# Kernel tuning notes

Measured on AMD Instinct MI355X. Metric: run time of the kernel, lower is better.

## Reference

```python
import jax, jax.numpy as jnp
import numpy as np

NUM_HEADS = 16
NUM_EXPERTS = 8
TOP_K = 2
LN_EPS = 1e-5


def _layernorm(x, g, b):
    mu = x.mean(-1, keepdims=True)
    var = ((x - mu) ** 2).mean(-1, keepdims=True)
    return (x - mu) * jax.lax.rsqrt(var + LN_EPS) * g + b


def _rope(x, cos, sin):
    # x: [B,S,H,D]; cos/sin: [S, D//2]; interleaved even/odd pairs
    B, S, H, D = x.shape
    xr = x.reshape(B, S, H, D // 2, 2)
    xe, xo = xr[..., 0], xr[..., 1]
    c = cos[None, :, None, :]
    s = sin[None, :, None, :]
    ye = xe * c - xo * s
    yo = xe * s + xo * c
    return jnp.stack((ye, yo), axis=-1).reshape(B, S, H, D)


def setup_inputs() -> dict:
    key = jax.random.key(0)
    ks = jax.random.split(key, 8)
    B, S, D = 4, 512, 1024
    E, Hd = NUM_EXPERTS, 1792
    sc = 0.02
    return {
        'x': jax.random.normal(ks[0], (B, S, D), jnp.float32),
        'ln1_g': jnp.ones((D,), jnp.float32),
        'ln1_b': jnp.zeros((D,), jnp.float32),
        'ln2_g': jnp.ones((D,), jnp.float32),
        'ln2_b': jnp.zeros((D,), jnp.float32),
        'w_qkv': jax.random.normal(ks[1], (D, 3 * D), jnp.float32) * sc,
        'w_o': jax.random.normal(ks[2], (D, D), jnp.float32) * sc,
        'gate_w': jax.random.normal(ks[3], (D, E), jnp.float32) * sc,
        'w_gate': jax.random.normal(ks[4], (E, D, Hd), jnp.float32) * sc,
        'w_up': jax.random.normal(ks[5], (E, D, Hd), jnp.float32) * sc,
        'w_down': jax.random.normal(ks[6], (E, Hd, D), jnp.float32) * sc,
    }


def reference(x, ln1_g, ln1_b, ln2_g, ln2_b, w_qkv, w_o, gate_w, w_gate, w_up, w_down):
    B, S, D = x.shape
    H = NUM_HEADS
    hd = D // H

    # --- attention with RoPE ---
    xn = _layernorm(x, ln1_g, ln1_b)
    qkv = xn @ w_qkv                      # [B,S,3D]
    q, k, v = jnp.split(qkv, 3, axis=-1)
    q = q.reshape(B, S, H, hd)
    k = k.reshape(B, S, H, hd)
    v = v.reshape(B, S, H, hd)
    inv_freq = 1.0 / (10000.0 ** (jnp.arange(0, hd, 2, dtype=jnp.float32) / hd))
    t = jnp.arange(S, dtype=jnp.float32)
    freqs = jnp.outer(t, inv_freq)        # [S, hd//2]
    cos, sin = jnp.cos(freqs), jnp.sin(freqs)
    q = _rope(q, cos, sin)
    k = _rope(k, cos, sin)
    scale = 1.0 / jnp.sqrt(jnp.asarray(hd, x.dtype))
    scores = jnp.einsum('bshd,bthd->bhst', q, k) * scale
    causal = jnp.tril(jnp.ones((S, S), bool))
    scores = jnp.where(causal[None, None], scores, jnp.finfo(scores.dtype).min)
    attn = jax.nn.softmax(scores, axis=-1)
    attn_out = jnp.einsum('bhst,bthd->bshd', attn, v).reshape(B, S, D)
    x = x + attn_out @ w_o

    # --- MoE ---
    xn2 = _layernorm(x, ln2_g, ln2_b)
    xf = xn2.reshape(-1, D)               # [T, D]
    logits = (xf.astype(jnp.bfloat16) @ gate_w.astype(jnp.bfloat16)).astype(jnp.float32)
    topk_w, topk_i = jax.lax.top_k(logits, TOP_K)
    topk_w = jax.nn.softmax(topk_w, axis=-1)
    probs = jax.nn.softmax(logits, axis=-1)
    expert_dist = probs.mean(0)
    lb_loss = NUM_EXPERTS * (expert_dist ** 2).sum()
    # dense dispatch: combine weights [T,E], zero where not selected (same math as sort/gather/scatter)
    cw = (jax.nn.one_hot(topk_i, NUM_EXPERTS, dtype=xf.dtype) * topk_w[..., None].astype(xf.dtype)).sum(1)
    g = jnp.einsum('td,edh->teh', xf, w_gate)
    u = jnp.einsum('td,edh->teh', xf, w_up)
    h = jax.nn.silu(g) * u
    down = jnp.einsum('teh,ehd->ted', h, w_down)
    moe_out = jnp.einsum('ted,te->td', down, cw).reshape(B, S, D)
    x = x + moe_out
    return (x, lb_loss, expert_dist)
```

## Files before the change

### kernel.cpp

```cpp
#include <hip/hip_runtime.h>
#include <hip/hip_bf16.h>
#include <math.h>

#define B_    4
#define S_    512
#define D_    1024
#define T_    2048
#define H_    16
#define HD_   64
#define E_    8
#define HID_  1792
#define D3_   3072
#define GU_   (2 * HID_)

typedef unsigned short ushort_t;
typedef __bf16 bf16x8 __attribute__((ext_vector_type(8)));
typedef float  floatx4 __attribute__((ext_vector_type(4)));

__device__ inline float bf2f(ushort_t u) {
    return __uint_as_float(((unsigned)u) << 16);
}
__device__ inline ushort_t f2bf(float f) {
    __hip_bfloat16 h = __float2bfloat16(f);
    return __builtin_bit_cast(ushort_t, h);
}

__device__ __forceinline__ void gl2lds16(const ushort_t* g, ushort_t* l) {
    __builtin_amdgcn_global_load_lds(
        (const __attribute__((address_space(1))) void*)g,
        (__attribute__((address_space(3))) void*)l, 16, 0, 0);
}

__global__ __launch_bounds__(256) void transpose_bf16_kernel(
    const float* __restrict__ in, ushort_t* __restrict__ out,
    int R, int C, int mul, int add, long outEstride)
{
    __shared__ float tile[32][33];
    const int bx = blockIdx.x * 32;
    const int by = blockIdx.y * 32;
    const size_t iofs = (size_t)blockIdx.z * R * C;
    const size_t oofs = (size_t)blockIdx.z * outEstride;
    const int tx = threadIdx.x & 31;
    const int ty = threadIdx.x >> 5;
#pragma unroll
    for (int i = 0; i < 4; i++) {
        int r = by + ty + i * 8;
        tile[ty + i * 8][tx] = in[iofs + (size_t)r * C + bx + tx];
    }
    __syncthreads();
#pragma unroll
    for (int i = 0; i < 4; i++) {
        int c = bx + ty + i * 8;
        out[oofs + (size_t)(c * mul + add) * R + by + tx] = f2bf(tile[tx][ty + i * 8]);
    }
}

__global__ __launch_bounds__(256) void ln_kernel(
    const float* __restrict__ x, const float* __restrict__ g,
    const float* __restrict__ b, float* __restrict__ outf,
    ushort_t* __restrict__ outb)
{
    const int t = blockIdx.x;
    const int tid = threadIdx.x;
    const int wave = tid >> 6, lane = tid & 63;
    const float4 v = ((const float4*)(x + (size_t)t * D_))[tid];

    float s = v.x + v.y + v.z + v.w;
#pragma unroll
    for (int off = 32; off; off >>= 1) s += __shfl_xor(s, off);
    __shared__ float red1[4];
    __shared__ float red2[4];
    if (lane == 0) red1[wave] = s;
    __syncthreads();
    const float mu = (red1[0] + red1[1] + red1[2] + red1[3]) * (1.0f / D_);

    const float dx = v.x - mu, dy = v.y - mu, dz = v.z - mu, dw = v.w - mu;
    float vs = dx * dx + dy * dy + dz * dz + dw * dw;
#pragma unroll
    for (int off = 32; off; off >>= 1) vs += __shfl_xor(vs, off);
    if (lane == 0) red2[wave] = vs;
    __syncthreads();
    const float var = (red2[0] + red2[1] + red2[2] + red2[3]) * (1.0f / D_);
    const float rs = 1.0f / sqrtf(var + 1e-5f);

    const float4 gg = ((const float4*)g)[tid];
    const float4 bb = ((const float4*)b)[tid];
    float4 o;
    o.x = dx * rs * gg.x + bb.x;
    o.y = dy * rs * gg.y + bb.y;
    o.z = dz * rs * gg.z + bb.z;
    o.w = dw * rs * gg.w + bb.w;
    if (outf) ((float4*)(outf + (size_t)t * D_))[tid] = o;
    if (outb) {
        ushort4 ob;
        ob.x = f2bf(o.x); ob.y = f2bf(o.y); ob.z = f2bf(o.z); ob.w = f2bf(o.w);
        ((ushort4*)(outb + (size_t)t * D_))[tid] = ob;
    }
}

template<int TM>
__global__ __launch_bounds__(256) void sgemm_kernel(
    const float* __restrict__ A, const float* __restrict__ B,
    const float* __restrict__ res, float* __restrict__ C,
    int M, int N, int K)
{
    constexpr int RM  = TM / 16;
    constexpr int TPR = 256 / TM;
    constexpr int KF  = 16 / TPR;
    __shared__ float As[16][TM + 4];
    __shared__ float Bs[16][68];
    const int tid = threadIdx.x;
    const int m0 = blockIdx.y * TM, n0 = blockIdx.x * 64;
    const int tx = tid & 15, ty = tid >> 4;

    float acc[RM][4] = {};

    const int arow = tid / TPR;
    const int akk  = (tid % TPR) * KF;
    const int bk = tid >> 4;
    const int bc = (tid & 15) * 4;

    const float* Ap = A + (size_t)(m0 + arow) * K + akk;
    const float* Bp = B + (size_t)bk * N + n0 + bc;

    for (int k0 = 0; k0 < K; k0 += 16) {
        float av[KF];
#pragma unroll
        for (int f = 0; f < KF / 4; f++) {
            const float4 t = *(const float4*)(Ap + k0 + f * 4);
            av[f * 4 + 0] = t.x; av[f * 4 + 1] = t.y;
            av[f * 4 + 2] = t.z; av[f * 4 + 3] = t.w;
        }
        const float4 bv = *(const float4*)(Bp + (size_t)k0 * N);
        __syncthreads();
#pragma unroll
        for (int i = 0; i < KF; i++) As[akk + i][arow] = av[i];
        *(float4*)&Bs[bk][bc] = bv;
        __syncthreads();
#pragma unroll
        for (int k = 0; k < 16; k++) {
            float a[RM];
#pragma unroll
            for (int f = 0; f < RM / 4; f++) {
                const float4 t = *(const float4*)&As[k][ty * RM + f * 4];
                a[f * 4 + 0] = t.x; a[f * 4 + 1] = t.y;
                a[f * 4 + 2] = t.z; a[f * 4 + 3] = t.w;
            }
            const float4 bb = *(const float4*)&Bs[k][tx * 4];
            const float bj[4] = {bb.x, bb.y, bb.z, bb.w};
#pragma unroll
            for (int i = 0; i < RM; i++)
#pragma unroll
                for (int j = 0; j < 4; j++)
                    acc[i][j] = fmaf(a[i], bj[j], acc[i][j]);
        }
    }

#pragma unroll
    for (int i = 0; i < RM; i++) {
        const int row = m0 + ty * RM + i;
        const size_t base = (size_t)row * N + n0 + tx * 4;
        float4 o;
        o.x = acc[i][0]; o.y = acc[i][1]; o.z = acc[i][2]; o.w = acc[i][3];
        if (res) {
            const float4 r0 = *(const float4*)(res + base);
            o.x += r0.x; o.y += r0.y; o.z += r0.z; o.w += r0.w;
        }
        *(float4*)(C + base) = o;
    }
}

__global__ __launch_bounds__(256) void gateup_idx_kernel(
    const ushort_t* __restrict__ A, const ushort_t* __restrict__ Bgu,
    const int* __restrict__ cnt, const int* __restrict__ tok,
    ushort_t* __restrict__ Hc)
{
    const int e = blockIdx.z;
    const int cntE = cnt[e];
    const int row0 = blockIdx.y * 128;
    if (row0 >= cntE) return;
    const int col0 = blockIdx.x * 128;
    const ushort_t* Bt = Bgu + (size_t)e * GU_ * D_;
    ushort_t* Hp = Hc + (size_t)e * T_ * HID_;

    __shared__ __align__(16) ushort_t As[128 * 32];
    __shared__ __align__(16) ushort_t Bs[128 * 32];
    const int tid = threadIdx.x, w = tid >> 6, lane = tid & 63;
    const int lr = lane >> 2, lc = (lane & 3) * 8;
    const int wm = (w >> 1) * 64, wn = (w & 1) * 64;
    const int lm = lane & 15, lq = lane >> 4;

    floatx4 acc[4][4] = {};

    int r0c = row0 + w * 16 + lr;  if (r0c > cntE - 1) r0c = cntE - 1;
    int r1c = row0 + 64 + w * 16 + lr; if (r1c > cntE - 1) r1c = cntE - 1;
    const ushort_t* Ap0 = A + (size_t)tok[e * T_ + r0c] * D_ + lc;
    const ushort_t* Ap1 = A + (size_t)tok[e * T_ + r1c] * D_ + lc;
    const ushort_t* Bp = Bt + (size_t)(col0 + w * 16 + lr) * D_ + lc;
    ushort_t* lA = As + w * 512;
    ushort_t* lB = Bs + w * 512;

    for (int k0 = 0; k0 < D_; k0 += 32) {
        __syncthreads();
        gl2lds16(Ap0 + k0, lA);
        gl2lds16(Ap1 + k0, lA + 2048);
        gl2lds16(Bp + k0, lB);
        gl2lds16(Bp + k0 + (size_t)64 * D_, lB + 2048);
        __syncthreads();
        bf16x8 a[4], b[4];
#pragma unroll
        for (int i = 0; i < 4; i++)
            a[i] = *(const bf16x8*)(As + (wm + i * 16 + lm) * 32 + lq * 8);
#pragma unroll
        for (int j = 0; j < 4; j++)
            b[j] = *(const bf16x8*)(Bs + (wn + j * 16 + lm) * 32 + lq * 8);
#pragma unroll
        for (int i = 0; i < 4; i++)
#pragma unroll
            for (int j = 0; j < 4; j++)
                acc[i][j] = __builtin_amdgcn_mfma_f32_16x16x32_bf16(a[i], b[j], acc[i][j], 0, 0, 0);
    }

#pragma unroll
    for (int i = 0; i < 4; i++)
#pragma unroll
        for (int j = 0; j < 4; j++)
#pragma unroll
            for (int r = 0; r < 4; r++) {
                const float v = acc[i][j][r];
                const float vp = __shfl_xor(v, 1);
                const float g = (lm & 1) ? vp : v;
                const float u = (lm & 1) ? v : vp;
                const float h = g / (1.f + __expf(-g)) * u;
                if (!(lm & 1)) {
                    const int row = row0 + wm + i * 16 + lq * 4 + r;
                    const int col = col0 + wn + j * 16 + lm;
                    Hp[(size_t)row * HID_ + (col >> 1)] = f2bf(h);
                }
            }
}

__global__ __launch_bounds__(256) void down_idx_kernel(
    const ushort_t* __restrict__ Hc, const ushort_t* __restrict__ Wd,
    const int* __restrict__ cnt, const int* __restrict__ tok,
    const float* __restrict__ wt, float* __restrict__ out)
{
    const int e = blockIdx.z;
    const int cntE = cnt[e];
    const int row0 = blockIdx.y * 128;
    if (row0 >= cntE) return;
    const int col0 = blockIdx.x * 128;
    const ushort_t* A = Hc + (size_t)e * T_ * HID_;
    const ushort_t* Bt = Wd + (size_t)e * D_ * HID_;

    __shared__ __align__(16) ushort_t As[128 * 32];
    __shared__ __align__(16) ushort_t Bs[128 * 32];
    const int tid = threadIdx.x, w = tid >> 6, lane = tid & 63;
    const int lr = lane >> 2, lc = (lane & 3) * 8;
    const int wm = (w >> 1) * 64, wn = (w & 1) * 64;
    const int lm = lane & 15, lq = lane >> 4;

    floatx4 acc[4][4] = {};

    const ushort_t* Ap = A + (size_t)(row0 + w * 16 + lr) * HID_ + lc;
    const ushort_t* Bp = Bt + (size_t)(col0 + w * 16 + lr) * HID_ + lc;
    ushort_t* lA = As + w * 512;
    ushort_t* lB = Bs + w * 512;

    for (int k0 = 0; k0 < HID_; k0 += 32) {
        __syncthreads();
        gl2lds16(Ap + k0, lA);
        gl2lds16(Ap + k0 + (size_t)64 * HID_, lA + 2048);
        gl2lds16(Bp + k0, lB);
        gl2lds16(Bp + k0 + (size_t)64 * HID_, lB + 2048);
        __syncthreads();
        bf16x8 a[4], b[4];
#pragma unroll
        for (int i = 0; i < 4; i++)
            a[i] = *(const bf16x8*)(As + (wm + i * 16 + lm) * 32 + lq * 8);
#pragma unroll
        for (int j = 0; j < 4; j++)
            b[j] = *(const bf16x8*)(Bs + (wn + j * 16 + lm) * 32 + lq * 8);
#pragma unroll
        for (int i = 0; i < 4; i++)
#pragma unroll
            for (int j = 0; j < 4; j++)
                acc[i][j] = __builtin_amdgcn_mfma_f32_16x16x32_bf16(a[i], b[j], acc[i][j], 0, 0, 0);
    }

#pragma unroll
    for (int i = 0; i < 4; i++)
#pragma unroll
        for (int r = 0; r < 4; r++) {
            const int row = row0 + wm + i * 16 + lq * 4 + r;
            if (row < cntE) {
                const int t = tok[e * T_ + row];
                const float scale = wt[e * T_ + row];
#pragma unroll
                for (int j = 0; j < 4; j++) {
                    const int col = col0 + wn + j * 16 + lm;
                    atomicAdd(&out[(size_t)t * D_ + col], scale * acc[i][j][r]);
                }
            }
        }
}

__global__ __launch_bounds__(256) void rope_table_kernel(
    float* __restrict__ ctab, float* __restrict__ stab)
{
    const int i = blockIdx.x * 256 + threadIdx.x;
    if (i >= S_ * 32) return;
    const int s = i >> 5, p = i & 31;
    const double e = (double)(2 * p) / 64.0;
    const float pf = (float)pow(10000.0, e);
    const float invf = 1.0f / pf;
    const float fr = (float)s * invf;
    ctab[i] = (float)cos((double)fr);
    stab[i] = (float)sin((double)fr);
}

__global__ __launch_bounds__(256) void rope_kernel(
    float* __restrict__ qkv, const float* __restrict__ ctab,
    const float* __restrict__ stab)
{
    const int n = blockIdx.x * 256 + threadIdx.x;
    const int pair = n & 31;
    const int h = (n >> 5) & 15;
    const int t = n >> 9;
    const int s = t & (S_ - 1);
    const float c = ctab[s * 32 + pair];
    const float sn = stab[s * 32 + pair];
    const size_t base = (size_t)t * D3_ + h * HD_ + pair * 2;
    float x0 = qkv[base], x1 = qkv[base + 1];
    qkv[base]     = x0 * c - x1 * sn;
    qkv[base + 1] = x0 * sn + x1 * c;
    x0 = qkv[base + D_]; x1 = qkv[base + D_ + 1];
    qkv[base + D_]     = x0 * c - x1 * sn;
    qkv[base + D_ + 1] = x0 * sn + x1 * c;
}

__global__ __launch_bounds__(256) void attn_kernel(
    const float* __restrict__ qkv, float* __restrict__ out)
{
    __shared__ float kbuf[64][65];
    __shared__ float vbuf[64][65];
    __shared__ float qs[32][64];
    __shared__ float ps[4][8][64];

    const int b = blockIdx.z, h = blockIdx.y, qt = blockIdx.x;
    const int tid = threadIdx.x, wave = tid >> 6, lane = tid & 63;
    const int q0 = qt * 32;

    for (int i = tid; i < 32 * 64; i += 256) {
        const int qi = i >> 6, d = i & 63;
        const int t = b * S_ + q0 + qi;
        qs[qi][d] = qkv[(size_t)t * D3_ + h * HD_ + d];
    }

    float m[8], l[8], O[8];
#pragma unroll
    for (int qi = 0; qi < 8; qi++) { m[qi] = -INFINITY; l[qi] = 0.f; O[qi] = 0.f; }

    const int maxS = q0 + 31;
    for (int c0 = 0; c0 <= maxS; c0 += 64) {
        __syncthreads();
        for (int i = tid; i < 64 * 16; i += 256) {
            const int key = i >> 4, d4 = (i & 15) * 4;
            const int t = b * S_ + c0 + key;
            const float4 kv = *(const float4*)(qkv + (size_t)t * D3_ + D_ + h * HD_ + d4);
            const float4 vv = *(const float4*)(qkv + (size_t)t * D3_ + 2 * D_ + h * HD_ + d4);
            kbuf[key][d4 + 0] = kv.x; kbuf[key][d4 + 1] = kv.y;
            kbuf[key][d4 + 2] = kv.z; kbuf[key][d4 + 3] = kv.w;
            vbuf[key][d4 + 0] = vv.x; vbuf[key][d4 + 1] = vv.y;
            vbuf[key][d4 + 2] = vv.z; vbuf[key][d4 + 3] = vv.w;
        }
        __syncthreads();

        const int kglob = c0 + lane;
        float sc[8];
#pragma unroll
        for (int qi = 0; qi < 8; qi++) sc[qi] = 0.f;
#pragma unroll 8
        for (int d = 0; d < 64; d++) {
            const float kv = kbuf[lane][d];
#pragma unroll
            for (int qi = 0; qi < 8; qi++)
                sc[qi] = fmaf(qs[wave * 8 + qi][d], kv, sc[qi]);
        }
#pragma unroll
        for (int qi = 0; qi < 8; qi++) {
            const int s = q0 + wave * 8 + qi;
            float v = (kglob <= s) ? sc[qi] * 0.125f : -INFINITY;
            float cmax = v;
#pragma unroll
            for (int off = 32; off; off >>= 1) cmax = fmaxf(cmax, __shfl_xor(cmax, off));
            const float mnew = fmaxf(m[qi], cmax);
            const float alpha = expf(m[qi] - mnew);
            const float p = (v == -INFINITY) ? 0.f : expf(v - mnew);
            float psum = p;
#pragma unroll
            for (int off = 32; off; off >>= 1) psum += __shfl_xor(psum, off);
            l[qi] = l[qi] * alpha + psum;
            m[qi] = mnew;
            ps[wave][qi][lane] = p;
            sc[qi] = alpha;
        }
#pragma unroll
        for (int qi = 0; qi < 8; qi++) O[qi] *= sc[qi];
#pragma unroll 8
        for (int j = 0; j < 64; j++) {
            const float vv = vbuf[j][lane];
#pragma unroll
            for (int qi = 0; qi < 8; qi++)
                O[qi] = fmaf(ps[wave][qi][j], vv, O[qi]);
        }
    }

#pragma unroll
    for (int qi = 0; qi < 8; qi++) {
        const int t = b * S_ + q0 + wave * 8 + qi;
        out[(size_t)t * D_ + h * HD_ + lane] = O[qi] / l[qi];
    }
}

__global__ __launch_bounds__(256) void copy_f32_kernel(
    const float* __restrict__ in, float* __restrict__ out, int n4)
{
    const int i = blockIdx.x * 256 + threadIdx.x;
    if (i < n4) ((float4*)out)[i] = ((const float4*)in)[i];
}

__global__ __launch_bounds__(64) void gate_kernel(
    const ushort_t* __restrict__ xn2, const float* __restrict__ gate_w,
    int* __restrict__ cnt, int* __restrict__ tok, float* __restrict__ wt,
    float* __restrict__ probs)
{
    const int t = blockIdx.x;
    const int lane = threadIdx.x;
    float acc[8] = {0, 0, 0, 0, 0, 0, 0, 0};
    for (int d = lane; d < D_; d += 64) {
        const float xv = bf2f(xn2[(size_t)t * D_ + d]);
        const float4 g0 = ((const float4*)(gate_w + d * 8))[0];
        const float4 g1 = ((const float4*)(gate_w + d * 8))[1];
        acc[0] = fmaf(xv, bf2f(f2bf(g0.x)), acc[0]);
        acc[1] = fmaf(xv, bf2f(f2bf(g0.y)), acc[1]);
        acc[2] = fmaf(xv, bf2f(f2bf(g0.z)), acc[2]);
        acc[3] = fmaf(xv, bf2f(f2bf(g0.w)), acc[3]);
        acc[4] = fmaf(xv, bf2f(f2bf(g1.x)), acc[4]);
        acc[5] = fmaf(xv, bf2f(f2bf(g1.y)), acc[5]);
        acc[6] = fmaf(xv, bf2f(f2bf(g1.z)), acc[6]);
        acc[7] = fmaf(xv, bf2f(f2bf(g1.w)), acc[7]);
    }
#pragma unroll
    for (int e = 0; e < 8; e++) {
#pragma unroll
        for (int off = 32; off; off >>= 1) acc[e] += __shfl_xor(acc[e], off);
        acc[e] = bf2f(f2bf(acc[e]));
    }

    if (lane == 0) {
        int i1 = 0;
        for (int e = 1; e < 8; e++) if (acc[e] > acc[i1]) i1 = e;
        int i2 = (i1 == 0) ? 1 : 0;
        for (int e = 0; e < 8; e++) if (e != i1 && acc[e] > acc[i2]) i2 = e;
        const float e2 = expf(acc[i2] - acc[i1]);
        const float w1 = 1.f / (1.f + e2);
        const float w2 = e2 * w1;
        const int p1 = atomicAdd(&cnt[i1], 1);
        tok[i1 * T_ + p1] = t; wt[i1 * T_ + p1] = w1;
        const int p2 = atomicAdd(&cnt[i2], 1);
        tok[i2 * T_ + p2] = t; wt[i2 * T_ + p2] = w2;
        const float mx = acc[i1];
        float se = 0.f, pe[8];
        for (int e = 0; e < 8; e++) { pe[e] = expf(acc[e] - mx); se += pe[e]; }
        const float inv = 1.f / se;
        for (int e = 0; e < 8; e++) probs[t * 8 + e] = pe[e] * inv;
    }
}

__global__ void zero_route_kernel(int* __restrict__ cnt)
{
    if (threadIdx.x < 8) cnt[threadIdx.x] = 0;
}

__global__ __launch_bounds__(256) void reduce_dist_kernel(
    const float* __restrict__ probs, float* __restrict__ out)
{
    __shared__ float part[256];
    __shared__ float dist8[8];
    const int tid = threadIdx.x;
    const int e = tid & 7, chunk = tid >> 3;
    float s = 0.f;
    for (int t = chunk; t < T_; t += 32) s += probs[t * 8 + e];
    part[tid] = s;
    __syncthreads();
    if (tid < 8) {
        float tot = 0.f;
        for (int c = 0; c < 32; c++) tot += part[c * 8 + tid];
        const float dv = tot * (1.0f / T_);
        dist8[tid] = dv;
        out[(size_t)T_ * D_ + 1 + tid] = dv;
    }
    __syncthreads();
    if (tid == 0) {
        float s2 = 0.f;
        for (int k = 0; k < 8; k++) s2 += dist8[k] * dist8[k];
        out[(size_t)T_ * D_] = (float)E_ * s2;
    }
}

extern "C" void kernel_launch(void* const* d_in, const int* in_sizes, int n_in,
                              void* d_out, int out_size, void* d_ws, size_t ws_size,
                              hipStream_t stream)
{
    const float* x      = (const float*)d_in[0];
    const float* ln1_g  = (const float*)d_in[1];
    const float* ln1_b  = (const float*)d_in[2];
    const float* ln2_g  = (const float*)d_in[3];
    const float* ln2_b  = (const float*)d_in[4];
    const float* w_qkv  = (const float*)d_in[5];
    const float* w_o    = (const float*)d_in[6];
    const float* gate_w = (const float*)d_in[7];
    const float* w_gate = (const float*)d_in[8];
    const float* w_up   = (const float*)d_in[9];
    const float* w_down = (const float*)d_in[10];
    float* out = (float*)d_out;

    char* ws = (char*)d_ws;
    size_t off = 0;
    auto alloc = [&](size_t bytes) { size_t o = off; off += (bytes + 255) & ~(size_t)255; return o; };
    ushort_t* wguT  = (ushort_t*)(ws + alloc((size_t)E_ * GU_ * D_ * 2));
    ushort_t* wdT   = (ushort_t*)(ws + alloc((size_t)E_ * D_ * HID_ * 2));
    float*    xn    = (float*)   (ws + alloc((size_t)T_ * D_ * 4));
    ushort_t* xn2   = (ushort_t*)(ws + alloc((size_t)T_ * D_ * 2));
    int*      cnt   = (int*)     (ws + alloc(64));
    int*      tok   = (int*)     (ws + alloc((size_t)E_ * T_ * 4));
    float*    wt    = (float*)   (ws + alloc((size_t)E_ * T_ * 4));
    float*    probs = (float*)   (ws + alloc((size_t)T_ * E_ * 4));
    float*    ctab  = (float*)   (ws + alloc((size_t)S_ * 32 * 4));
    float*    stab  = (float*)   (ws + alloc((size_t)S_ * 32 * 4));
    const size_t scratch0 = alloc((size_t)E_ * T_ * HID_ * 2);
    float*    qkv   = (float*)   (ws + scratch0);
    float*    attnO = (float*)   (ws + scratch0 + (size_t)T_ * D3_ * 4);
    float*    x1    = (float*)   (ws + scratch0 + (size_t)T_ * D3_ * 4 + (size_t)T_ * D_ * 4);
    ushort_t* Hc    = (ushort_t*)(ws + scratch0);
    (void)ws_size; (void)in_sizes; (void)n_in; (void)out_size;

    hipLaunchKernelGGL(transpose_bf16_kernel, dim3(HID_ / 32, D_ / 32, E_), dim3(256), 0, stream,
                       w_gate, wguT, D_, HID_, 2, 0, (long)GU_ * D_);
    hipLaunchKernelGGL(transpose_bf16_kernel, dim3(HID_ / 32, D_ / 32, E_), dim3(256), 0, stream,
                       w_up, wguT, D_, HID_, 2, 1, (long)GU_ * D_);
    hipLaunchKernelGGL(transpose_bf16_kernel, dim3(D_ / 32, HID_ / 32, E_), dim3(256), 0, stream,
                       w_down, wdT, HID_, D_, 1, 0, (long)D_ * HID_);

    hipLaunchKernelGGL(rope_table_kernel, dim3((S_ * 32 + 255) / 256), dim3(256), 0, stream,
                       ctab, stab);

    hipLaunchKernelGGL(ln_kernel, dim3(T_), dim3(256), 0, stream,
                       x, ln1_g, ln1_b, xn, (ushort_t*)nullptr);

    hipLaunchKernelGGL((sgemm_kernel<128>), dim3(D3_ / 64, T_ / 128), dim3(256), 0, stream,
                       xn, w_qkv, (const float*)nullptr, qkv, T_, D3_, D_);

    hipLaunchKernelGGL(rope_kernel, dim3(T_ * H_ * 32 / 256), dim3(256), 0, stream,
                       qkv, ctab, stab);

    hipLaunchKernelGGL(attn_kernel, dim3(S_ / 32, H_, B_), dim3(256), 0, stream, qkv, attnO);

    hipLaunchKernelGGL((sgemm_kernel<64>), dim3(D_ / 64, T_ / 64), dim3(256), 0, stream,
                       attnO, w_o, x, x1, T_, D_, D_);

    hipLaunchKernelGGL(copy_f32_kernel, dim3(T_ * D_ / 4 / 256), dim3(256), 0, stream,
                       x1, out, T_ * D_ / 4);

    hipLaunchKernelGGL(ln_kernel, dim3(T_), dim3(256), 0, stream,
                       x1, ln2_g, ln2_b, (float*)nullptr, xn2);

    hipLaunchKernelGGL(zero_route_kernel, dim3(1), dim3(64), 0, stream, cnt);
    hipLaunchKernelGGL(gate_kernel, dim3(T_), dim3(64), 0, stream,
                       xn2, gate_w, cnt, tok, wt, probs);
    hipLaunchKernelGGL(reduce_dist_kernel, dim3(1), dim3(256), 0, stream, probs, out);

    hipLaunchKernelGGL(gateup_idx_kernel, dim3(GU_ / 128, T_ / 128, E_), dim3(256), 0, stream,
                       xn2, wguT, cnt, tok, Hc);
    hipLaunchKernelGGL(down_idx_kernel, dim3(D_ / 128, T_ / 128, E_), dim3(256), 0, stream,
                       Hc, wdT, cnt, tok, wt, out);
}
```

Measured before the change: 838.5 us.

## Fuse residual copy into O-proj GEMM, vectorize attention LDS reads, reverse tile order

The output-projection GEMM now writes its result to a second destination directly, which removes the separate copy kernel and its extra read and write of the activation. The attention kernel reads K, Q and P from shared memory as float4, padding the K buffer to 68 columns for alignment, so fewer LDS instructions are issued in the inner loops. Query tiles are also launched in reverse order so the longest causal blocks start first, which should balance the tail. The main risk is LDS bank conflicts from the wider accesses.

```diff
diff --git a/kernel.cpp b/kernel.cpp
--- a/kernel.cpp
+++ b/kernel.cpp
@@ -102,7 +102,7 @@
 __global__ __launch_bounds__(256) void sgemm_kernel(
     const float* __restrict__ A, const float* __restrict__ B,
     const float* __restrict__ res, float* __restrict__ C,
-    int M, int N, int K)
+    float* __restrict__ C2, int M, int N, int K)
 {
     constexpr int RM  = TM / 16;
     constexpr int TPR = 256 / TM;
@@ -167,6 +167,7 @@
             o.x += r0.x; o.y += r0.y; o.z += r0.z; o.w += r0.w;
         }
         *(float4*)(C + base) = o;
+        if (C2) *(float4*)(C2 + base) = o;
     }
 }
 
@@ -342,12 +343,13 @@
 __global__ __launch_bounds__(256) void attn_kernel(
     const float* __restrict__ qkv, float* __restrict__ out)
 {
-    __shared__ float kbuf[64][65];
+    __shared__ __align__(16) float kbuf[64][68];
     __shared__ float vbuf[64][65];
-    __shared__ float qs[32][64];
-    __shared__ float ps[4][8][64];
-
-    const int b = blockIdx.z, h = blockIdx.y, qt = blockIdx.x;
+    __shared__ __align__(16) float qs[32][64];
+    __shared__ __align__(16) float ps[4][8][64];
+
+    const int b = blockIdx.z, h = blockIdx.y;
+    const int qt = (int)gridDim.x - 1 - (int)blockIdx.x;
     const int tid = threadIdx.x, wave = tid >> 6, lane = tid & 63;
     const int q0 = qt * 32;
 
@@ -365,14 +367,13 @@
     for (int c0 = 0; c0 <= maxS; c0 += 64) {
         __syncthreads();
         for (int i = tid; i < 64 * 16; i += 256) {
-            const int key = i >> 4, d4 = (i & 15) * 4;
+            const int key = i >> 4, g = i & 15;
             const int t = b * S_ + c0 + key;
-            const float4 kv = *(const float4*)(qkv + (size_t)t * D3_ + D_ + h * HD_ + d4);
-            const float4 vv = *(const float4*)(qkv + (size_t)t * D3_ + 2 * D_ + h * HD_ + d4);
-            kbuf[key][d4 + 0] = kv.x; kbuf[key][d4 + 1] = kv.y;
-            kbuf[key][d4 + 2] = kv.z; kbuf[key][d4 + 3] = kv.w;
-            vbuf[key][d4 + 0] = vv.x; vbuf[key][d4 + 1] = vv.y;
-            vbuf[key][d4 + 2] = vv.z; vbuf[key][d4 + 3] = vv.w;
+            const float4 kv = *(const float4*)(qkv + (size_t)t * D3_ + D_ + h * HD_ + g * 4);
+            const float4 vv = *(const float4*)(qkv + (size_t)t * D3_ + 2 * D_ + h * HD_ + g * 4);
+            *(float4*)&kbuf[key][g * 4] = kv;
+            vbuf[key][g * 4 + 0] = vv.x; vbuf[key][g * 4 + 1] = vv.y;
+            vbuf[key][g * 4 + 2] = vv.z; vbuf[key][g * 4 + 3] = vv.w;
         }
         __syncthreads();
 
@@ -380,12 +381,19 @@
         float sc[8];
 #pragma unroll
         for (int qi = 0; qi < 8; qi++) sc[qi] = 0.f;
-#pragma unroll 8
-        for (int d = 0; d < 64; d++) {
-            const float kv = kbuf[lane][d];
-#pragma unroll
-            for (int qi = 0; qi < 8; qi++)
-                sc[qi] = fmaf(qs[wave * 8 + qi][d], kv, sc[qi]);
+#pragma unroll 4
+        for (int g = 0; g < 16; g++) {
+            const float4 kv = *(const float4*)&kbuf[lane][g * 4];
+#pragma unroll
+            for (int qi = 0; qi < 8; qi++) {
+                const float4 qv = *(const float4*)&qs[wave * 8 + qi][g * 4];
+                float s = sc[qi];
+                s = fmaf(qv.x, kv.x, s);
+                s = fmaf(qv.y, kv.y, s);
+                s = fmaf(qv.z, kv.z, s);
+                s = fmaf(qv.w, kv.w, s);
+                sc[qi] = s;
+            }
         }
 #pragma unroll
         for (int qi = 0; qi < 8; qi++) {
@@ -407,12 +415,22 @@
         }
 #pragma unroll
         for (int qi = 0; qi < 8; qi++) O[qi] *= sc[qi];
-#pragma unroll 8
-        for (int j = 0; j < 64; j++) {
-            const float vv = vbuf[j][lane];
-#pragma unroll
-            for (int qi = 0; qi < 8; qi++)
-                O[qi] = fmaf(ps[wave][qi][j], vv, O[qi]);
+#pragma unroll 4
+        for (int g = 0; g < 16; g++) {
+            const float v0 = vbuf[g * 4 + 0][lane];
+            const float v1 = vbuf[g * 4 + 1][lane];
+            const float v2 = vbuf[g * 4 + 2][lane];
+            const float v3 = vbuf[g * 4 + 3][lane];
+#pragma unroll
+            for (int qi = 0; qi < 8; qi++) {
+                const float4 p4 = *(const float4*)&ps[wave][qi][g * 4];
+                float o = O[qi];
+                o = fmaf(p4.x, v0, o);
+                o = fmaf(p4.y, v1, o);
+                o = fmaf(p4.z, v2, o);
+                o = fmaf(p4.w, v3, o);
+                O[qi] = o;
+            }
         }
     }
 
@@ -421,13 +439,6 @@
         const int t = b * S_ + q0 + wave * 8 + qi;
         out[(size_t)t * D_ + h * HD_ + lane] = O[qi] / l[qi];
     }
-}
-
-__global__ __launch_bounds__(256) void copy_f32_kernel(
-    const float* __restrict__ in, float* __restrict__ out, int n4)
-{
-    const int i = blockIdx.x * 256 + threadIdx.x;
-    if (i < n4) ((float4*)out)[i] = ((const float4*)in)[i];
 }
 
 __global__ __launch_bounds__(64) void gate_kernel(
@@ -560,7 +571,7 @@
                        x, ln1_g, ln1_b, xn, (ushort_t*)nullptr);
 
     hipLaunchKernelGGL((sgemm_kernel<128>), dim3(D3_ / 64, T_ / 128), dim3(256), 0, stream,
-                       xn, w_qkv, (const float*)nullptr, qkv, T_, D3_, D_);
+                       xn, w_qkv, (const float*)nullptr, qkv, (float*)nullptr, T_, D3_, D_);
 
     hipLaunchKernelGGL(rope_kernel, dim3(T_ * H_ * 32 / 256), dim3(256), 0, stream,
                        qkv, ctab, stab);
@@ -568,10 +579,7 @@
     hipLaunchKernelGGL(attn_kernel, dim3(S_ / 32, H_, B_), dim3(256), 0, stream, qkv, attnO);
 
     hipLaunchKernelGGL((sgemm_kernel<64>), dim3(D_ / 64, T_ / 64), dim3(256), 0, stream,
-                       attnO, w_o, x, x1, T_, D_, D_);
-
-    hipLaunchKernelGGL(copy_f32_kernel, dim3(T_ * D_ / 4 / 256), dim3(256), 0, stream,
-                       x1, out, T_ * D_ / 4);
+                       attnO, w_o, x, x1, out, T_, D_, D_);
 
     hipLaunchKernelGGL(ln_kernel, dim3(T_), dim3(256), 0, stream,
                        x1, ln2_g, ln2_b, (float*)nullptr, xn2);
```

After: 857.3 us. 2.2% more time.
